# Kernel optimization log

Measured on AMD Instinct MI355X. Metric: run time of the kernel, lower is better.

## Reference

```python
import jax, jax.numpy as jnp
import numpy as np

MARGIN = 0.1


def setup_inputs() -> dict:
    key = jax.random.key(0)
    k1, k2 = jax.random.split(key)
    scores = jax.random.normal(k1, (32, 2048), dtype=jnp.float32)
    labels = jax.random.randint(k2, (32, 2048), 0, 2, dtype=jnp.int32)
    return {"scores": scores, "labels": labels}


def reference(scores, labels):
    # scores: [B, N] float, labels: [B, N] in {0, 1}
    pos = labels == 1  # [B, N]
    neg = labels == 0  # [B, N]
    # pairwise hinge: relu(margin - pos_score_i + neg_score_j), masked to (pos, neg) pairs
    hinge = jnp.maximum(MARGIN - scores[:, :, None] + scores[:, None, :], 0.0)  # [B, N, N]
    pair_mask = pos[:, :, None] & neg[:, None, :]  # [B, N, N]
    row_sum = jnp.sum(jnp.where(pair_mask, hinge, 0.0), axis=(1, 2))  # [B]
    n_pairs = pos.sum(axis=1).astype(scores.dtype) * neg.sum(axis=1).astype(scores.dtype)  # [B]
    valid = n_pairs > 0  # rows with both pos and neg (others skipped in torch loop)
    row_loss = row_sum / jnp.maximum(n_pairs, 1.0)  # per-row pairwise mean
    n_valid = valid.sum().astype(scores.dtype)
    total = jnp.sum(jnp.where(valid, row_loss, 0.0)) / jnp.maximum(n_valid, 1.0)
    # if no valid rows, torch returns 0.0
    return jnp.where(n_valid > 0, total, jnp.asarray(0.0, scores.dtype))
```

## Files before the change

kernel.cpp:

```cpp
#include <hip/hip_runtime.h>


#define MARGIN   0.1f
#define BROWS    32
#define NCOLS    2048
#define THREADS  256
#define J_SPLIT  16
#define JCHUNK   (NCOLS / J_SPLIT)
#define NPART    J_SPLIT
#define KMAX     (NCOLS / THREADS)


template<int KC>
__device__ __forceinline__ void main_loop(const float* __restrict__ tneg,
                                          const float* __restrict__ c,
                                          float* __restrict__ acc)
{
    const float4* t4 = (const float4*)tneg;
    #pragma unroll
    for (int j8 = 0; j8 < JCHUNK / 8; ++j8) {
        const float4 v0 = t4[2 * j8];
        const float4 v1 = t4[2 * j8 + 1];
        #pragma unroll
        for (int k = 0; k < KC; ++k) {
            const float ck = c[k];
            acc[0] += fmaxf(ck + v0.x, 0.f);
            acc[1] += fmaxf(ck + v0.y, 0.f);
            acc[2] += fmaxf(ck + v0.z, 0.f);
            acc[3] += fmaxf(ck + v0.w, 0.f);
            acc[4] += fmaxf(ck + v1.x, 0.f);
            acc[5] += fmaxf(ck + v1.y, 0.f);
            acc[6] += fmaxf(ck + v1.z, 0.f);
            acc[7] += fmaxf(ck + v1.w, 0.f);
        }
    }
}

__global__ __launch_bounds__(THREADS) void rank_pair_kernel(
    const float* __restrict__ scores, const int* __restrict__ labels,
    float* __restrict__ ws)
{
    const int jb = blockIdx.x;
    const int b  = blockIdx.y;

    __shared__ float tneg[JCHUNK];
    __shared__ float clist[NCOLS];
    __shared__ int   cnt_pos;
    __shared__ float wsum[THREADS / 64];

    const float* srow = scores + (size_t)b * NCOLS;
    const int*   lrow = labels + (size_t)b * NCOLS;
    const int tid  = threadIdx.x;
    const int lane = tid & 63;
    const int wave = tid >> 6;

    if (tid == 0) cnt_pos = 0;
    __syncthreads();

    if (tid < JCHUNK) {
        const int gj = jb * JCHUNK + tid;
        const float s = srow[gj];
        tneg[tid] = (lrow[gj] == 0) ? s : -1e30f;
    }

    #pragma unroll
    for (int it = 0; it < KMAX; ++it) {
        const int idx = it * THREADS + tid;
        const float s = srow[idx];
        const bool ispos = (lrow[idx] == 1);
        const unsigned long long mask = __ballot(ispos);
        int base = 0;
        if (lane == 0) base = atomicAdd(&cnt_pos, (int)__popcll(mask));
        base = __shfl(base, 0, 64);
        if (ispos) {
            const int off = (int)__popcll(mask & ((1ull << lane) - 1ull));
            clist[base + off] = MARGIN - s;
        }
    }
    __syncthreads();

    const int P = cnt_pos;

    float c[KMAX];
    #pragma unroll
    for (int k = 0; k < KMAX; ++k) {
        const int r = k * THREADS + tid;
        c[k] = (r < P) ? clist[r] : -1e30f;
    }
    const int kcap = (P + THREADS - 1) / THREADS;

    float acc[8] = {0.f, 0.f, 0.f, 0.f, 0.f, 0.f, 0.f, 0.f};
    switch (kcap) {
        case 1: main_loop<1>(tneg, c, acc); break;
        case 2: main_loop<2>(tneg, c, acc); break;
        case 3: main_loop<3>(tneg, c, acc); break;
        case 4: main_loop<4>(tneg, c, acc); break;
        case 5: main_loop<5>(tneg, c, acc); break;
        case 6: main_loop<6>(tneg, c, acc); break;
        case 7: main_loop<7>(tneg, c, acc); break;
        case 8: main_loop<8>(tneg, c, acc); break;
        default: break;
    }
    float a = ((acc[0] + acc[1]) + (acc[2] + acc[3]))
            + ((acc[4] + acc[5]) + (acc[6] + acc[7]));

    #pragma unroll
    for (int off = 32; off >= 1; off >>= 1)
        a += __shfl_down(a, off, 64);
    if (lane == 0) wsum[wave] = a;
    __syncthreads();

    if (tid == 0) {
        float tot = 0.f;
        #pragma unroll
        for (int w = 0; w < THREADS / 64; ++w) tot += wsum[w];
        ws[(size_t)b * NPART + jb] = tot;
        if (jb == 0)
            ((int*)ws)[BROWS * NPART + b] = P;
    }
}

__global__ __launch_bounds__(64) void rank_finalize_kernel(
    const float* __restrict__ ws, float* __restrict__ out)
{
    const int t = threadIdx.x;
    float loss = 0.f, valid = 0.f;
    if (t < BROWS) {
        float s = 0.f;
        #pragma unroll
        for (int p = 0; p < NPART; ++p) s += ws[t * NPART + p];
        const int np = ((const int*)ws)[BROWS * NPART + t];
        const int nn = NCOLS - np;
        const float pairs = (float)np * (float)nn;
        if (pairs > 0.f) { valid = 1.f; loss = s / pairs; }
    }
    #pragma unroll
    for (int off = 32; off >= 1; off >>= 1) {
        loss  += __shfl_down(loss,  off, 64);
        valid += __shfl_down(valid, off, 64);
    }
    if (t == 0) out[0] = (valid > 0.f) ? (loss / valid) : 0.f;
}

extern "C" void kernel_launch(void* const* d_in, const int* in_sizes, int n_in,
                              void* d_out, int out_size, void* d_ws, size_t ws_size,
                              hipStream_t stream)
{
    const float* scores = (const float*)d_in[0];
    const int*   labels = (const int*)d_in[1];
    float* out = (float*)d_out;
    float* ws  = (float*)d_ws;

    dim3 grid(J_SPLIT, BROWS);
    rank_pair_kernel<<<grid, THREADS, 0, stream>>>(scores, labels, ws);
    rank_finalize_kernel<<<1, 64, 0, stream>>>(ws, out);
}
```

Before: 15.62 us.

## Fuse finalize into pair kernel via cooperative grid sync; vectorize positive compaction

```diff
diff --git a/kernel.cpp b/kernel.cpp
--- a/kernel.cpp
+++ b/kernel.cpp
@@ -1,10 +1,14 @@
 #include <hip/hip_runtime.h>
+#include <hip/hip_cooperative_groups.h>
+
+namespace cg = cooperative_groups;
 
 
 #define MARGIN   0.1f
 #define BROWS    32
 #define NCOLS    2048
 #define THREADS  256
+#define NWAVES   (THREADS / 64)
 #define J_SPLIT  16
 #define JCHUNK   (NCOLS / J_SPLIT)
 #define NPART    J_SPLIT
@@ -36,17 +40,17 @@
     }
 }
 
-__global__ __launch_bounds__(THREADS) void rank_pair_kernel(
+__global__ __launch_bounds__(THREADS, 2) void rank_fused_kernel(
     const float* __restrict__ scores, const int* __restrict__ labels,
-    float* __restrict__ ws)
+    float* __restrict__ ws, float* __restrict__ out)
 {
     const int jb = blockIdx.x;
     const int b  = blockIdx.y;
 
     __shared__ float tneg[JCHUNK];
     __shared__ float clist[NCOLS];
-    __shared__ int   cnt_pos;
-    __shared__ float wsum[THREADS / 64];
+    __shared__ int   wcnt[NWAVES];
+    __shared__ float wsum[NWAVES];
 
     const float* srow = scores + (size_t)b * NCOLS;
     const int*   lrow = labels + (size_t)b * NCOLS;
@@ -54,32 +58,43 @@
     const int lane = tid & 63;
     const int wave = tid >> 6;
 
-    if (tid == 0) cnt_pos = 0;
-    __syncthreads();
-
     if (tid < JCHUNK) {
         const int gj = jb * JCHUNK + tid;
         const float s = srow[gj];
         tneg[tid] = (lrow[gj] == 0) ? s : -1e30f;
     }
 
+    const float4 s0 = ((const float4*)srow)[tid * 2];
+    const float4 s1 = ((const float4*)srow)[tid * 2 + 1];
+    const int4   l0 = ((const int4*)lrow)[tid * 2];
+    const int4   l1 = ((const int4*)lrow)[tid * 2 + 1];
+    const float v[8] = {s0.x, s0.y, s0.z, s0.w, s1.x, s1.y, s1.z, s1.w};
+    const int   lb[8] = {l0.x, l0.y, l0.z, l0.w, l1.x, l1.y, l1.z, l1.w};
+
+    int mycnt = 0;
     #pragma unroll
-    for (int it = 0; it < KMAX; ++it) {
-        const int idx = it * THREADS + tid;
-        const float s = srow[idx];
-        const bool ispos = (lrow[idx] == 1);
-        const unsigned long long mask = __ballot(ispos);
-        int base = 0;
-        if (lane == 0) base = atomicAdd(&cnt_pos, (int)__popcll(mask));
-        base = __shfl(base, 0, 64);
-        if (ispos) {
-            const int off = (int)__popcll(mask & ((1ull << lane) - 1ull));
-            clist[base + off] = MARGIN - s;
-        }
+    for (int k = 0; k < 8; ++k) mycnt += (lb[k] == 1);
+
+    int scan = mycnt;
+    #pragma unroll
+    for (int off = 1; off < 64; off <<= 1) {
+        const int n = __shfl_up(scan, off, 64);
+        if (lane >= off) scan += n;
     }
+    if (lane == 63) wcnt[wave] = scan;
     __syncthreads();
 
-    const int P = cnt_pos;
+    int wbase = 0, P = 0;
+    #pragma unroll
+    for (int w = 0; w < NWAVES; ++w) {
+        P += wcnt[w];
+        if (w < wave) wbase += wcnt[w];
+    }
+    int pos = wbase + (scan - mycnt);
+    #pragma unroll
+    for (int k = 0; k < 8; ++k)
+        if (lb[k] == 1) clist[pos++] = MARGIN - v[k];
+    __syncthreads();
 
     float c[KMAX];
     #pragma unroll
@@ -113,33 +128,32 @@
     if (tid == 0) {
         float tot = 0.f;
         #pragma unroll
-        for (int w = 0; w < THREADS / 64; ++w) tot += wsum[w];
+        for (int w = 0; w < NWAVES; ++w) tot += wsum[w];
         ws[(size_t)b * NPART + jb] = tot;
         if (jb == 0)
             ((int*)ws)[BROWS * NPART + b] = P;
     }
-}
 
-__global__ __launch_bounds__(64) void rank_finalize_kernel(
-    const float* __restrict__ ws, float* __restrict__ out)
-{
-    const int t = threadIdx.x;
-    float loss = 0.f, valid = 0.f;
-    if (t < BROWS) {
-        float s = 0.f;
+    cg::this_grid().sync();
+
+    if (blockIdx.x == 0 && blockIdx.y == 0 && tid < 64) {
+        float loss = 0.f, valid = 0.f;
+        if (tid < BROWS) {
+            float s = 0.f;
+            #pragma unroll
+            for (int p = 0; p < NPART; ++p) s += ws[tid * NPART + p];
+            const int np = ((const int*)ws)[BROWS * NPART + tid];
+            const int nn = NCOLS - np;
+            const float pairs = (float)np * (float)nn;
+            if (pairs > 0.f) { valid = 1.f; loss = s / pairs; }
+        }
         #pragma unroll
-        for (int p = 0; p < NPART; ++p) s += ws[t * NPART + p];
-        const int np = ((const int*)ws)[BROWS * NPART + t];
-        const int nn = NCOLS - np;
-        const float pairs = (float)np * (float)nn;
-        if (pairs > 0.f) { valid = 1.f; loss = s / pairs; }
+        for (int off = 32; off >= 1; off >>= 1) {
+            loss  += __shfl_down(loss,  off, 64);
+            valid += __shfl_down(valid, off, 64);
+        }
+        if (tid == 0) out[0] = (valid > 0.f) ? (loss / valid) : 0.f;
     }
-    #pragma unroll
-    for (int off = 32; off >= 1; off >>= 1) {
-        loss  += __shfl_down(loss,  off, 64);
-        valid += __shfl_down(valid, off, 64);
-    }
-    if (t == 0) out[0] = (valid > 0.f) ? (loss / valid) : 0.f;
 }
 
 extern "C" void kernel_launch(void* const* d_in, const int* in_sizes, int n_in,
@@ -151,7 +165,8 @@
     float* out = (float*)d_out;
     float* ws  = (float*)d_ws;
 
-    dim3 grid(J_SPLIT, BROWS);
-    rank_pair_kernel<<<grid, THREADS, 0, stream>>>(scores, labels, ws);
-    rank_finalize_kernel<<<1, 64, 0, stream>>>(ws, out);
+    void* args[] = { (void*)&scores, (void*)&labels, (void*)&ws, (void*)&out };
+    dim3 grid(J_SPLIT, BROWS), block(THREADS);
+    hipLaunchCooperativeKernel((const void*)rank_fused_kernel,
+                               grid, block, args, 0, stream);
 }
```

Result: slower. 60.91 us (+289.9%).
